# Optimization experiments

Hardware: AMD Instinct MI355X
Metric: run time of the kernel (lower is better)

The kernel has to match this reference:

```python
import jax, jax.numpy as jnp
import numpy as np

N_NODES = 100000
N_EDGES = 1600000
IN_F = 128
HID = 128
OUT_F = 40


def _gcn_conv(x, W, b, src, dst):
    # PyG GCNConv: h = x @ W; out[dst] += norm * h[src]; out += b
    n = x.shape[0]
    h = x @ W  # [N, out_channels]
    deg = jnp.zeros((n,), h.dtype).at[dst].add(jnp.ones((dst.shape[0],), h.dtype))
    dinv = jnp.where(deg > 0, jax.lax.rsqrt(deg), 0.0)  # deg^{-1/2}
    norm = dinv[src] * dinv[dst]  # [E+N]
    msg = h[src] * norm[:, None]  # [E+N, out_channels] gather
    out = jnp.zeros_like(h).at[dst].add(msg)  # scatter-add at targets
    if b is not None:
        out = out + b
    return out


def setup_inputs() -> dict:
    key = jax.random.key(0)
    k_x, k_e, k1, k2, k3, kb1, kb2 = jax.random.split(key, 7)
    x = jax.random.normal(k_x, (N_NODES, IN_F), dtype=jnp.float32)
    edge_index = jax.random.randint(k_e, (2, N_EDGES), 0, N_NODES, dtype=jnp.int64)
    s_in = 1.0 / np.sqrt(IN_F)
    s_h = 1.0 / np.sqrt(HID)
    W_in = jax.random.normal(k1, (IN_F, HID), dtype=jnp.float32) * s_in
    b_in = jnp.zeros((HID,), dtype=jnp.float32)
    W_mid = jax.random.normal(k2, (HID, HID), dtype=jnp.float32) * s_h
    b_mid = jnp.zeros((HID,), dtype=jnp.float32)
    W_out = jax.random.normal(k3, (HID, OUT_F), dtype=jnp.float32) * s_h
    return {"x": x, "edge_index": edge_index, "W_in": W_in, "b_in": b_in,
            "W_mid": W_mid, "b_mid": b_mid, "W_out": W_out}


def reference(x, edge_index, W_in, b_in, W_mid, b_mid, W_out):
    n = x.shape[0]
    loops = jnp.arange(n, dtype=edge_index.dtype)
    src = jnp.concatenate([edge_index[0], loops])  # add self-loops
    dst = jnp.concatenate([edge_index[1], loops])
    h = jax.nn.relu(_gcn_conv(x, W_in, b_in, src, dst))
    h = jax.nn.relu(_gcn_conv(h, W_mid, b_mid, src, dst))
    h = _gcn_conv(h, W_out, None, src, dst)  # out_conv: bias=False
    return jax.nn.log_softmax(h, axis=1)
```

## Files before the change

### kernel.cpp

```cpp
#include <hip/hip_runtime.h>
#include <math.h>

#define N_NODES 100000
#define N_EDGES 1600000
#define NBUCK 391
#define BSTRIDE 4608

typedef __attribute__((ext_vector_type(8))) _Float16 h8v;
typedef __attribute__((ext_vector_type(4))) float f32x4;
typedef __attribute__((ext_vector_type(2))) int i32x2;


__launch_bounds__(256)
__global__ void k_prep(const int* __restrict__ srcv, const int* __restrict__ dstv,
                       int* __restrict__ bcnt, unsigned int* __restrict__ ebuf,
                       const float* __restrict__ W1, const float* __restrict__ W2,
                       const float* __restrict__ W3, _Float16* __restrict__ Wt,
                       _Float16* __restrict__ bufA, _Float16* __restrict__ bufB,
                       _Float16* __restrict__ zbuf) {
    const int tid = threadIdx.x;
    const int bid = blockIdx.x;

    if (bid >= 391) {
        if (bid == 543) {
            if (tid < 128) {
                bufA[(size_t)N_NODES * 128 + tid] = (_Float16)0.f;
                bufB[(size_t)N_NODES * 128 + tid] = (_Float16)0.f;
            }
            if (tid < 64)  zbuf[(size_t)N_NODES * 64 + tid] = (_Float16)0.f;
            return;
        }
        int idx = (bid - 391) * 256 + tid;
        if (idx >= 304 * 128) return;
        int n = idx / 128, k = idx % 128;
        const float* W;
        int ncols, nloc;
        _Float16 *ph, *pl;
        if (n < 128)      { W = W1; ncols = 128; nloc = n;       ph = Wt;                 pl = Wt + 128 * 128; }
        else if (n < 256) { W = W2; ncols = 128; nloc = n - 128; ph = Wt + 2 * 128 * 128; pl = Wt + 3 * 128 * 128; }
        else              { W = W3; ncols = 40;  nloc = n - 256; ph = Wt + 4 * 128 * 128; pl = Wt + 4 * 128 * 128 + 48 * 128; }
        float v = (nloc < ncols) ? W[k * ncols + nloc] : 0.f;
        _Float16 hi = (_Float16)v;
        _Float16 lo = (_Float16)(v - (float)hi);
        ph[nloc * 128 + k] = hi;
        pl[nloc * 128 + k] = lo;
        return;
    }

    __shared__ int hist[NBUCK];
    __shared__ int cur[NBUCK];
    for (int t = tid; t < NBUCK; t += 256) hist[t] = 0;
    __syncthreads();
    const int base = bid * 4096;
#pragma unroll
    for (int i = 0; i < 16; i++) {
        int e = base + i * 256 + tid;
        if (e < N_EDGES) atomicAdd(&hist[dstv[e] >> 8], 1);
    }
    __syncthreads();
    for (int t = tid; t < NBUCK; t += 256)
        if (hist[t]) cur[t] = t * BSTRIDE + atomicAdd(&bcnt[t], hist[t]);
    __syncthreads();
#pragma unroll
    for (int i = 0; i < 16; i++) {
        int e = base + i * 256 + tid;
        if (e < N_EDGES) {
            int d = dstv[e];
            int p = atomicAdd(&cur[d >> 8], 1);
            ebuf[p] = ((unsigned int)srcv[e] << 8) | (unsigned int)(d & 255);
        }
    }
}

__launch_bounds__(256)
__global__ void k_bucket(const unsigned int* __restrict__ ebuf, const int* __restrict__ bcnt,
                         i32x2* __restrict__ rowse, float* __restrict__ dinv,
                         int* __restrict__ colidx) {
    __shared__ int cnt[256];
    __shared__ int s[256];
    __shared__ int cur[256];
    const int tid = threadIdx.x;
    const int b = blockIdx.x;
    const int e0 = b * BSTRIDE;
    const int e1 = e0 + bcnt[b];
    cnt[tid] = 0;
    __syncthreads();
    for (int e = e0 + tid; e < e1; e += 256) atomicAdd(&cnt[ebuf[e] & 255u], 1);
    __syncthreads();
    int v = cnt[tid];
    int x = v;
    s[tid] = x;
    __syncthreads();
    for (int d = 1; d < 256; d <<= 1) {
        int t = (tid >= d) ? s[tid - d] : 0;
        __syncthreads();
        x += t;
        s[tid] = x;
        __syncthreads();
    }
    int start = e0 + x - v;
    int node = b * 256 + tid;
    if (node < N_NODES) {
        i32x2 se;
        se.x = start;
        se.y = start + v;
        rowse[node] = se;
        dinv[node] = rsqrtf((float)(v + 1));
    }
    cur[tid] = start;
    __syncthreads();
    for (int e = e0 + tid; e < e1; e += 256) {
        unsigned int sd = ebuf[e];
        int pos = atomicAdd(&cur[sd & 255u], 1);
        colidx[pos] = (int)(sd >> 8);
    }
}


#define GEMM_GRID 625
#define NTILES 3125

__launch_bounds__(256, 2)
__global__ void k_gemm128_f32(const float* __restrict__ Af,
                              const _Float16* __restrict__ Wthi, const _Float16* __restrict__ Wtlo,
                              const float* __restrict__ dinv, _Float16* __restrict__ out) {
    const int lane = threadIdx.x & 63;
    const int wi = threadIdx.x >> 6;
    const int nb = wi * 32;
    const int nn = lane & 15;
    const int kq = (lane >> 4) * 8;
    const int quad = lane >> 4;

    h8v bh[4][2], bl[4][2];
#pragma unroll
    for (int c = 0; c < 4; c++)
#pragma unroll
        for (int t = 0; t < 2; t++) {
            int off = (nb + t * 16 + nn) * 128 + c * 32 + kq;
            bh[c][t] = *(const h8v*)(Wthi + off);
            bl[c][t] = *(const h8v*)(Wtlo + off);
        }

    for (int rt = blockIdx.x; rt < NTILES; rt += GEMM_GRID) {
        const int r0 = rt * 32;
        f32x4 acc[2][2] = {};
#pragma unroll
        for (int c = 0; c < 4; c++) {
            h8v a[2];
#pragma unroll
            for (int m = 0; m < 2; m++) {
                const float* p = Af + (size_t)(r0 + m * 16 + nn) * 128 + c * 32 + kq;
                float4 p0 = *(const float4*)p;
                float4 p1 = *(const float4*)(p + 4);
                h8v av = {(_Float16)p0.x, (_Float16)p0.y, (_Float16)p0.z, (_Float16)p0.w,
                          (_Float16)p1.x, (_Float16)p1.y, (_Float16)p1.z, (_Float16)p1.w};
                a[m] = av;
            }
#pragma unroll
            for (int m = 0; m < 2; m++)
#pragma unroll
                for (int t = 0; t < 2; t++) {
                    acc[m][t] = __builtin_amdgcn_mfma_f32_16x16x32_f16(a[m], bh[c][t], acc[m][t], 0, 0, 0);
                    acc[m][t] = __builtin_amdgcn_mfma_f32_16x16x32_f16(a[m], bl[c][t], acc[m][t], 0, 0, 0);
                }
        }
#pragma unroll
        for (int m = 0; m < 2; m++)
#pragma unroll
            for (int reg = 0; reg < 4; reg++) {
                int r = r0 + m * 16 + quad * 4 + reg;
                float dv = dinv[r];
#pragma unroll
                for (int t = 0; t < 2; t++)
                    out[(size_t)r * 128 + nb + t * 16 + nn] = (_Float16)(acc[m][t][reg] * dv);
            }
    }
}


__launch_bounds__(256, 2)
__global__ void k_fused128(const _Float16* __restrict__ hp, const i32x2* __restrict__ rowse,
                           const int* __restrict__ colidx, const float* __restrict__ bias,
                           const float* __restrict__ dinv,
                           const _Float16* __restrict__ Wthi, const _Float16* __restrict__ Wtlo,
                           _Float16* __restrict__ out) {
    __shared__ __align__(16) _Float16 As[32 * 128];
    const int lane = threadIdx.x & 63;
    const int wi = threadIdx.x >> 6;
    const int nn = lane & 15;
    const int quad = lane >> 4;
    const int kq = quad * 8;
    const int nb = wi * 32;

    h8v bh[4][2], bl[4][2];
#pragma unroll
    for (int c = 0; c < 4; c++)
#pragma unroll
        for (int t = 0; t < 2; t++) {
            int off = (nb + t * 16 + nn) * 128 + c * 32 + kq;
            bh[c][t] = *(const h8v*)(Wthi + off);
            bl[c][t] = *(const h8v*)(Wtlo + off);
        }

    const int r0 = blockIdx.x * 32;

    const int rs = quad;
    const int cp = nn;
    const _Float16* hpc = hp + cp * 8;
    const float* bp = bias + cp * 8;
    float4 b0 = *(const float4*)bp;
    float4 b1 = *(const float4*)(bp + 4);
    float bb[8] = {b0.x, b0.y, b0.z, b0.w, b1.x, b1.y, b1.z, b1.w};
#pragma unroll
    for (int p = 0; p < 2; p++) {
        const int rl = wi * 8 + p * 4 + rs;
        const int r = r0 + rl;
        const i32x2 se = rowse[r];
        const int deg = se.y - se.x;
        int m = deg;
        m = max(m, __shfl_xor(m, 16));
        m = max(m, __shfl_xor(m, 32));
        h8v acc = {};
        for (int it = 0; it < m; it += 4) {
            int i0 = se.x + it;
            int s0 = colidx[i0];
            int s1 = colidx[i0 + 1];
            int s2 = colidx[i0 + 2];
            int s3 = colidx[i0 + 3];
            s0 = (it < deg) ? s0 : N_NODES;
            s1 = (it + 1 < deg) ? s1 : N_NODES;
            s2 = (it + 2 < deg) ? s2 : N_NODES;
            s3 = (it + 3 < deg) ? s3 : N_NODES;
            h8v v0 = *(const h8v*)(hpc + (size_t)s0 * 128);
            h8v v1 = *(const h8v*)(hpc + (size_t)s1 * 128);
            h8v v2 = *(const h8v*)(hpc + (size_t)s2 * 128);
            h8v v3 = *(const h8v*)(hpc + (size_t)s3 * 128);
            acc += v0;
            acc += v1;
            acc += v2;
            acc += v3;
        }
        h8v sv = *(const h8v*)(hpc + (size_t)r * 128);
        float dv = rsqrtf((float)(deg + 1));
        h8v o;
#pragma unroll
        for (int j = 0; j < 8; j++) {
            float sx = (float)acc[j] + (float)sv[j];
            o[j] = (_Float16)fmaxf(fmaf(dv, sx, bb[j]), 0.f);
        }
        *(h8v*)(As + rl * 128 + ((cp ^ (rl & 15)) * 8)) = o;
    }
    __syncthreads();

    f32x4 acc2[2][2] = {};
#pragma unroll
    for (int c = 0; c < 4; c++) {
        h8v a[2];
#pragma unroll
        for (int mm = 0; mm < 2; mm++) {
            int R = mm * 16 + nn;
            int ch = (c * 4 + quad) ^ (R & 15);
            a[mm] = *(const h8v*)(As + R * 128 + ch * 8);
        }
#pragma unroll
        for (int mm = 0; mm < 2; mm++)
#pragma unroll
            for (int t = 0; t < 2; t++) {
                acc2[mm][t] = __builtin_amdgcn_mfma_f32_16x16x32_f16(a[mm], bh[c][t], acc2[mm][t], 0, 0, 0);
                acc2[mm][t] = __builtin_amdgcn_mfma_f32_16x16x32_f16(a[mm], bl[c][t], acc2[mm][t], 0, 0, 0);
            }
    }
#pragma unroll
    for (int mm = 0; mm < 2; mm++)
#pragma unroll
        for (int reg = 0; reg < 4; reg++) {
            int r = r0 + mm * 16 + quad * 4 + reg;
            float dv = dinv[r];
#pragma unroll
            for (int t = 0; t < 2; t++)
                out[(size_t)r * 128 + nb + t * 16 + nn] = (_Float16)(acc2[mm][t][reg] * dv);
        }
}

__launch_bounds__(256, 2)
__global__ void k_fused40(const _Float16* __restrict__ hp, const i32x2* __restrict__ rowse,
                          const int* __restrict__ colidx, const float* __restrict__ bias,
                          const float* __restrict__ dinv,
                          const _Float16* __restrict__ Wthi, const _Float16* __restrict__ Wtlo,
                          _Float16* __restrict__ out) {
    __shared__ __align__(16) _Float16 As[32 * 128];
    const int lane = threadIdx.x & 63;
    const int wi = threadIdx.x >> 6;
    const int nn = lane & 15;
    const int quad = lane >> 4;
    const int kq = quad * 8;

    h8v bh[4], bl[4];
    if (wi < 3) {
#pragma unroll
        for (int c = 0; c < 4; c++) {
            int off = (wi * 16 + nn) * 128 + c * 32 + kq;
            bh[c] = *(const h8v*)(Wthi + off);
            bl[c] = *(const h8v*)(Wtlo + off);
        }
    }

    const int r0 = blockIdx.x * 32;

    const int rs = quad;
    const int cp = nn;
    const _Float16* hpc = hp + cp * 8;
    const float* bp = bias + cp * 8;
    float4 b0 = *(const float4*)bp;
    float4 b1 = *(const float4*)(bp + 4);
    float bb[8] = {b0.x, b0.y, b0.z, b0.w, b1.x, b1.y, b1.z, b1.w};
#pragma unroll
    for (int p = 0; p < 2; p++) {
        const int rl = wi * 8 + p * 4 + rs;
        const int r = r0 + rl;
        const i32x2 se = rowse[r];
        const int deg = se.y - se.x;
        int m = deg;
        m = max(m, __shfl_xor(m, 16));
        m = max(m, __shfl_xor(m, 32));
        h8v acc = {};
        for (int it = 0; it < m; it += 4) {
            int i0 = se.x + it;
            int s0 = colidx[i0];
            int s1 = colidx[i0 + 1];
            int s2 = colidx[i0 + 2];
            int s3 = colidx[i0 + 3];
            s0 = (it < deg) ? s0 : N_NODES;
            s1 = (it + 1 < deg) ? s1 : N_NODES;
            s2 = (it + 2 < deg) ? s2 : N_NODES;
            s3 = (it + 3 < deg) ? s3 : N_NODES;
            h8v v0 = *(const h8v*)(hpc + (size_t)s0 * 128);
            h8v v1 = *(const h8v*)(hpc + (size_t)s1 * 128);
            h8v v2 = *(const h8v*)(hpc + (size_t)s2 * 128);
            h8v v3 = *(const h8v*)(hpc + (size_t)s3 * 128);
            acc += v0;
            acc += v1;
            acc += v2;
            acc += v3;
        }
        h8v sv = *(const h8v*)(hpc + (size_t)r * 128);
        float dv = rsqrtf((float)(deg + 1));
        h8v o;
#pragma unroll
        for (int j = 0; j < 8; j++) {
            float sx = (float)acc[j] + (float)sv[j];
            o[j] = (_Float16)fmaxf(fmaf(dv, sx, bb[j]), 0.f);
        }
        *(h8v*)(As + rl * 128 + ((cp ^ (rl & 15)) * 8)) = o;
    }
    __syncthreads();

    if (wi < 3) {
        f32x4 acc2[2] = {};
#pragma unroll
        for (int c = 0; c < 4; c++) {
            h8v a[2];
#pragma unroll
            for (int mm = 0; mm < 2; mm++) {
                int R = mm * 16 + nn;
                int ch = (c * 4 + quad) ^ (R & 15);
                a[mm] = *(const h8v*)(As + R * 128 + ch * 8);
            }
#pragma unroll
            for (int mm = 0; mm < 2; mm++) {
                acc2[mm] = __builtin_amdgcn_mfma_f32_16x16x32_f16(a[mm], bh[c], acc2[mm], 0, 0, 0);
                acc2[mm] = __builtin_amdgcn_mfma_f32_16x16x32_f16(a[mm], bl[c], acc2[mm], 0, 0, 0);
            }
        }
#pragma unroll
        for (int mm = 0; mm < 2; mm++)
#pragma unroll
            for (int reg = 0; reg < 4; reg++) {
                int r = r0 + mm * 16 + quad * 4 + reg;
                float dv = dinv[r];
                out[(size_t)r * 64 + wi * 16 + nn] = (_Float16)(acc2[mm][reg] * dv);
            }
    }
}


__launch_bounds__(256)
__global__ void k_agg_out(const _Float16* __restrict__ hp, const i32x2* __restrict__ rowse,
                          const int* __restrict__ colidx, float* __restrict__ out) {
    const int lane = threadIdx.x & 63;
    const int wid = (blockIdx.x * blockDim.x + threadIdx.x) >> 6;
    const int rs = lane >> 3;
    const int cp = lane & 7;
    const int r = wid * 8 + rs;

    const i32x2 se = rowse[r];
    const int deg = se.y - se.x;
    int m = deg;
    m = max(m, __shfl_xor(m, 8));
    m = max(m, __shfl_xor(m, 16));
    m = max(m, __shfl_xor(m, 32));

    const _Float16* hpc = hp + cp * 8;
    h8v acc = {};
    for (int it = 0; it < m; it += 4) {
        int i0 = se.x + it;
        int s0 = colidx[i0];
        int s1 = colidx[i0 + 1];
        int s2 = colidx[i0 + 2];
        int s3 = colidx[i0 + 3];
        s0 = (it < deg) ? s0 : N_NODES;
        s1 = (it + 1 < deg) ? s1 : N_NODES;
        s2 = (it + 2 < deg) ? s2 : N_NODES;
        s3 = (it + 3 < deg) ? s3 : N_NODES;
        h8v v0 = *(const h8v*)(hpc + (size_t)s0 * 64);
        h8v v1 = *(const h8v*)(hpc + (size_t)s1 * 64);
        h8v v2 = *(const h8v*)(hpc + (size_t)s2 * 64);
        h8v v3 = *(const h8v*)(hpc + (size_t)s3 * 64);
        acc += v0;
        acc += v1;
        acc += v2;
        acc += v3;
    }

    h8v sv = *(const h8v*)(hpc + (size_t)r * 64);
    float dv = rsqrtf((float)(deg + 1));
    float z[8];
#pragma unroll
    for (int j = 0; j < 8; j++) z[j] = dv * ((float)acc[j] + (float)sv[j]);

    const bool act = cp < 5;
    float pm = -INFINITY;
    if (act) {
#pragma unroll
        for (int j = 0; j < 8; j++) pm = fmaxf(pm, z[j]);
    }
    pm = fmaxf(pm, __shfl_xor(pm, 1));
    pm = fmaxf(pm, __shfl_xor(pm, 2));
    pm = fmaxf(pm, __shfl_xor(pm, 4));
    float pe = 0.f;
    if (act) {
#pragma unroll
        for (int j = 0; j < 8; j++) pe += __expf(z[j] - pm);
    }
    pe += __shfl_xor(pe, 1);
    pe += __shfl_xor(pe, 2);
    pe += __shfl_xor(pe, 4);
    float lse = __logf(pe);
    if (act) {
        float* po = out + (size_t)r * 40 + cp * 8;
        float4 o0 = make_float4(z[0] - pm - lse, z[1] - pm - lse, z[2] - pm - lse, z[3] - pm - lse);
        float4 o1 = make_float4(z[4] - pm - lse, z[5] - pm - lse, z[6] - pm - lse, z[7] - pm - lse);
        *(float4*)po = o0;
        *(float4*)(po + 4) = o1;
    }
}


extern "C" void kernel_launch(void* const* d_in, const int* in_sizes, int n_in,
                              void* d_out, int out_size, void* d_ws, size_t ws_size,
                              hipStream_t stream) {
    const float* x     = (const float*)d_in[0];
    const int*   ei    = (const int*)d_in[1];
    const float* W_in  = (const float*)d_in[2];
    const float* b_in  = (const float*)d_in[3];
    const float* W_mid = (const float*)d_in[4];
    const float* b_mid = (const float*)d_in[5];
    const float* W_out = (const float*)d_in[6];
    float* out = (float*)d_out;

    const int* srcv = ei;
    const int* dstv = ei + N_EDGES;

    char* w = (char*)d_ws;
    float* dinv   = (float*)(w);
    i32x2* rowse  = (i32x2*)(w + (1ull << 19));
    int* bcnt     = (int*)(w + 1507328);
    int* colidx   = (int*)(w + (2ull << 20));
    unsigned int* ebuf = (unsigned int*)(w + (10ull << 20));
    _Float16* Wt  = (_Float16*)(w + (18ull << 20));
    _Float16* bufA = (_Float16*)(w + (19ull << 20));
    _Float16* bufB = (_Float16*)(w + (45ull << 20));
    _Float16* zbuf = (_Float16*)(w + (71ull << 20));

    _Float16* W1h = Wt;
    _Float16* W1l = Wt + 128 * 128;
    _Float16* W2h = Wt + 2 * 128 * 128;
    _Float16* W2l = Wt + 3 * 128 * 128;
    _Float16* W3h = Wt + 4 * 128 * 128;
    _Float16* W3l = Wt + 4 * 128 * 128 + 48 * 128;

    (void)hipMemsetAsync(bcnt, 0, NBUCK * sizeof(int), stream);
    k_prep<<<544, 256, 0, stream>>>(srcv, dstv, bcnt, ebuf, W_in, W_mid, W_out, Wt, bufA, bufB, zbuf);
    k_bucket<<<NBUCK, 256, 0, stream>>>(ebuf, bcnt, rowse, dinv, colidx);

    k_gemm128_f32<<<GEMM_GRID, 256, 0, stream>>>(x, W1h, W1l, dinv, bufA);
    k_fused128<<<NTILES, 256, 0, stream>>>(bufA, rowse, colidx, b_in, dinv, W2h, W2l, bufB);
    k_fused40<<<NTILES, 256, 0, stream>>>(bufB, rowse, colidx, b_mid, dinv, W3h, W3l, zbuf);
    k_agg_out<<<N_NODES / 32, 256, 0, stream>>>(zbuf, rowse, colidx, out);
}
```

Before: 353.0 us.

## Fold first-layer GEMM into prep kernel and move source scaling into aggregation

The first-layer GEMM on x no longer depends on degree normalisation, so it is merged into the prep kernel as extra blocks. It runs alongside edge bucketing, and one kernel launch is removed. Source-side dinv scaling now happens inside the gather loops, with fp32 accumulation and a zeroed dinv sentinel, instead of in the GEMM epilogues. The fused kernels now use 16-row tiles with weights loaded per block instead of held in registers. This gives more blocks and lower register pressure, at the cost of extra dinv gathers per edge and repeated weight loads.

```diff
diff --git a/kernel.cpp b/kernel.cpp
--- a/kernel.cpp
+++ b/kernel.cpp
@@ -10,19 +10,80 @@
 typedef __attribute__((ext_vector_type(4))) float f32x4;
 typedef __attribute__((ext_vector_type(2))) int i32x2;
 
-
-__launch_bounds__(256)
+#define GEMM_GRID 625
+#define NTILES 3125
+
+
 __global__ void k_prep(const int* __restrict__ srcv, const int* __restrict__ dstv,
                        int* __restrict__ bcnt, unsigned int* __restrict__ ebuf,
-                       const float* __restrict__ W1, const float* __restrict__ W2,
-                       const float* __restrict__ W3, _Float16* __restrict__ Wt,
+                       const float* __restrict__ x, const float* __restrict__ W1,
+                       const float* __restrict__ W2, const float* __restrict__ W3,
+                       _Float16* __restrict__ Wt,
                        _Float16* __restrict__ bufA, _Float16* __restrict__ bufB,
                        _Float16* __restrict__ zbuf) {
     const int tid = threadIdx.x;
     const int bid = blockIdx.x;
 
-    if (bid >= 391) {
-        if (bid == 543) {
+    if (bid < 625) {
+        const int lane = tid & 63;
+        const int wi = tid >> 6;
+        const int nb = wi * 32;
+        const int nn = lane & 15;
+        const int quad = lane >> 4;
+        const int kq = quad * 8;
+
+        h8v bh[4][2], bl[4][2];
+#pragma unroll
+        for (int c = 0; c < 4; c++)
+#pragma unroll
+            for (int t = 0; t < 2; t++) {
+#pragma unroll
+                for (int j = 0; j < 8; j++) {
+                    float w = W1[(c * 32 + kq + j) * 128 + nb + t * 16 + nn];
+                    _Float16 hi = (_Float16)w;
+                    bh[c][t][j] = hi;
+                    bl[c][t][j] = (_Float16)(w - (float)hi);
+                }
+            }
+
+        for (int rt = bid; rt < NTILES; rt += GEMM_GRID) {
+            const int r0 = rt * 32;
+            f32x4 acc[2][2] = {};
+#pragma unroll
+            for (int c = 0; c < 4; c++) {
+                h8v a[2];
+#pragma unroll
+                for (int m = 0; m < 2; m++) {
+                    const float* p = x + (size_t)(r0 + m * 16 + nn) * 128 + c * 32 + kq;
+                    float4 p0 = *(const float4*)p;
+                    float4 p1 = *(const float4*)(p + 4);
+                    h8v av = {(_Float16)p0.x, (_Float16)p0.y, (_Float16)p0.z, (_Float16)p0.w,
+                              (_Float16)p1.x, (_Float16)p1.y, (_Float16)p1.z, (_Float16)p1.w};
+                    a[m] = av;
+                }
+#pragma unroll
+                for (int m = 0; m < 2; m++)
+#pragma unroll
+                    for (int t = 0; t < 2; t++) {
+                        acc[m][t] = __builtin_amdgcn_mfma_f32_16x16x32_f16(a[m], bh[c][t], acc[m][t], 0, 0, 0);
+                        acc[m][t] = __builtin_amdgcn_mfma_f32_16x16x32_f16(a[m], bl[c][t], acc[m][t], 0, 0, 0);
+                    }
+            }
+#pragma unroll
+            for (int m = 0; m < 2; m++)
+#pragma unroll
+                for (int reg = 0; reg < 4; reg++) {
+                    int r = r0 + m * 16 + quad * 4 + reg;
+#pragma unroll
+                    for (int t = 0; t < 2; t++)
+                        bufA[(size_t)r * 128 + nb + t * 16 + nn] = (_Float16)acc[m][t][reg];
+                }
+        }
+        return;
+    }
+
+    if (bid >= 1016) {
+        if (bid == 1104) {
             if (tid < 128) {
                 bufA[(size_t)N_NODES * 128 + tid] = (_Float16)0.f;
                 bufB[(size_t)N_NODES * 128 + tid] = (_Float16)0.f;
@@ -30,20 +91,24 @@
             if (tid < 64)  zbuf[(size_t)N_NODES * 64 + tid] = (_Float16)0.f;
             return;
         }
-        int idx = (bid - 391) * 256 + tid;
-        if (idx >= 304 * 128) return;
+        int idx = (bid - 1016) * 256 + tid;
+        if (idx >= 176 * 128) return;
         int n = idx / 128, k = idx % 128;
-        const float* W;
-        int ncols, nloc;
         _Float16 *ph, *pl;
-        if (n < 128)      { W = W1; ncols = 128; nloc = n;       ph = Wt;                 pl = Wt + 128 * 128; }
-        else if (n < 256) { W = W2; ncols = 128; nloc = n - 128; ph = Wt + 2 * 128 * 128; pl = Wt + 3 * 128 * 128; }
-        else              { W = W3; ncols = 40;  nloc = n - 256; ph = Wt + 4 * 128 * 128; pl = Wt + 4 * 128 * 128 + 48 * 128; }
-        float v = (nloc < ncols) ? W[k * ncols + nloc] : 0.f;
+        float v;
+        if (n < 128) {
+            v = W2[k * 128 + n];
+            ph = Wt + 2 * 128 * 128; pl = Wt + 3 * 128 * 128;
+        } else {
+            int nloc = n - 128;
+            v = (nloc < 40) ? W3[k * 40 + nloc] : 0.f;
+            ph = Wt + 4 * 128 * 128; pl = Wt + 4 * 128 * 128 + 48 * 128;
+            n = nloc;
+        }
         _Float16 hi = (_Float16)v;
         _Float16 lo = (_Float16)(v - (float)hi);
-        ph[nloc * 128 + k] = hi;
-        pl[nloc * 128 + k] = lo;
+        ph[n * 128 + k] = hi;
+        pl[n * 128 + k] = lo;
         return;
     }
 
@@ -51,7 +116,7 @@
     __shared__ int cur[NBUCK];
     for (int t = tid; t < NBUCK; t += 256) hist[t] = 0;
     __syncthreads();
-    const int base = bid * 4096;
+    const int base = (bid - 625) * 4096;
 #pragma unroll
     for (int i = 0; i < 16; i++) {
         int e = base + i * 256 + tid;
@@ -81,6 +146,7 @@
     __shared__ int cur[256];
     const int tid = threadIdx.x;
     const int b = blockIdx.x;
+    if (b == 0 && tid == 0) dinv[N_NODES] = 0.f;
     const int e0 = b * BSTRIDE;
     const int e1 = e0 + bcnt[b];
     cnt[tid] = 0;
@@ -117,110 +183,29 @@
 }
 
 
-#define GEMM_GRID 625
-#define NTILES 3125
-
-__launch_bounds__(256, 2)
-__global__ void k_gemm128_f32(const float* __restrict__ Af,
-                              const _Float16* __restrict__ Wthi, const _Float16* __restrict__ Wtlo,
-                              const float* __restrict__ dinv, _Float16* __restrict__ out) {
-    const int lane = threadIdx.x & 63;
-    const int wi = threadIdx.x >> 6;
-    const int nb = wi * 32;
-    const int nn = lane & 15;
-    const int kq = (lane >> 4) * 8;
-    const int quad = lane >> 4;
-
-    h8v bh[4][2], bl[4][2];
-#pragma unroll
-    for (int c = 0; c < 4; c++)
-#pragma unroll
-        for (int t = 0; t < 2; t++) {
-            int off = (nb + t * 16 + nn) * 128 + c * 32 + kq;
-            bh[c][t] = *(const h8v*)(Wthi + off);
-            bl[c][t] = *(const h8v*)(Wtlo + off);
-        }
-
-    for (int rt = blockIdx.x; rt < NTILES; rt += GEMM_GRID) {
-        const int r0 = rt * 32;
-        f32x4 acc[2][2] = {};
-#pragma unroll
-        for (int c = 0; c < 4; c++) {
-            h8v a[2];
-#pragma unroll
-            for (int m = 0; m < 2; m++) {
-                const float* p = Af + (size_t)(r0 + m * 16 + nn) * 128 + c * 32 + kq;
-                float4 p0 = *(const float4*)p;
-                float4 p1 = *(const float4*)(p + 4);
-                h8v av = {(_Float16)p0.x, (_Float16)p0.y, (_Float16)p0.z, (_Float16)p0.w,
-                          (_Float16)p1.x, (_Float16)p1.y, (_Float16)p1.z, (_Float16)p1.w};
-                a[m] = av;
-            }
-#pragma unroll
-            for (int m = 0; m < 2; m++)
-#pragma unroll
-                for (int t = 0; t < 2; t++) {
-                    acc[m][t] = __builtin_amdgcn_mfma_f32_16x16x32_f16(a[m], bh[c][t], acc[m][t], 0, 0, 0);
-                    acc[m][t] = __builtin_amdgcn_mfma_f32_16x16x32_f16(a[m], bl[c][t], acc[m][t], 0, 0, 0);
-                }
-        }
-#pragma unroll
-        for (int m = 0; m < 2; m++)
-#pragma unroll
-            for (int reg = 0; reg < 4; reg++) {
-                int r = r0 + m * 16 + quad * 4 + reg;
-                float dv = dinv[r];
-#pragma unroll
-                for (int t = 0; t < 2; t++)
-                    out[(size_t)r * 128 + nb + t * 16 + nn] = (_Float16)(acc[m][t][reg] * dv);
-            }
-    }
-}
-
-
-__launch_bounds__(256, 2)
+__launch_bounds__(256)
 __global__ void k_fused128(const _Float16* __restrict__ hp, const i32x2* __restrict__ rowse,
                            const int* __restrict__ colidx, const float* __restrict__ bias,
                            const float* __restrict__ dinv,
                            const _Float16* __restrict__ Wthi, const _Float16* __restrict__ Wtlo,
                            _Float16* __restrict__ out) {
-    __shared__ __align__(16) _Float16 As[32 * 128];
+    __shared__ __align__(16) _Float16 As[16 * 128];
     const int lane = threadIdx.x & 63;
     const int wi = threadIdx.x >> 6;
     const int nn = lane & 15;
     const int quad = lane >> 4;
-    const int kq = quad * 8;
-    const int nb = wi * 32;
-
-    h8v bh[4][2], bl[4][2];
-#pragma unroll
-    for (int c = 0; c < 4; c++)
-#pragma unroll
-        for (int t = 0; t < 2; t++) {
-            int off = (nb + t * 16 + nn) * 128 + c * 32 + kq;
-            bh[c][t] = *(const h8v*)(Wthi + off);
-            bl[c][t] = *(const h8v*)(Wtlo + off);
-        }
-
-    const int r0 = blockIdx.x * 32;
-
-    const int rs = quad;
-    const int cp = nn;
-    const _Float16* hpc = hp + cp * 8;
-    const float* bp = bias + cp * 8;
-    float4 b0 = *(const float4*)bp;
-    float4 b1 = *(const float4*)(bp + 4);
-    float bb[8] = {b0.x, b0.y, b0.z, b0.w, b1.x, b1.y, b1.z, b1.w};
-#pragma unroll
-    for (int p = 0; p < 2; p++) {
-        const int rl = wi * 8 + p * 4 + rs;
+    const int r0 = blockIdx.x * 16;
+
+    {
+        const int rl = wi * 4 + quad;
         const int r = r0 + rl;
         const i32x2 se = rowse[r];
         const int deg = se.y - se.x;
         int m = deg;
         m = max(m, __shfl_xor(m, 16));
         m = max(m, __shfl_xor(m, 32));
-        h8v acc = {};
+        const _Float16* hpc = hp + nn * 8;
+        float accf[8] = {};
         for (int it = 0; it < m; it += 4) {
             int i0 = se.x + it;
             int s0 = colidx[i0];
@@ -231,99 +216,86 @@
             s1 = (it + 1 < deg) ? s1 : N_NODES;
             s2 = (it + 2 < deg) ? s2 : N_NODES;
             s3 = (it + 3 < deg) ? s3 : N_NODES;
+            float d0 = dinv[s0];
+            float d1 = dinv[s1];
+            float d2 = dinv[s2];
+            float d3 = dinv[s3];
             h8v v0 = *(const h8v*)(hpc + (size_t)s0 * 128);
             h8v v1 = *(const h8v*)(hpc + (size_t)s1 * 128);
             h8v v2 = *(const h8v*)(hpc + (size_t)s2 * 128);
             h8v v3 = *(const h8v*)(hpc + (size_t)s3 * 128);
-            acc += v0;
-            acc += v1;
-            acc += v2;
-            acc += v3;
+#pragma unroll
+            for (int j = 0; j < 8; j++) {
+                accf[j] = fmaf(d0, (float)v0[j], accf[j]);
+                accf[j] = fmaf(d1, (float)v1[j], accf[j]);
+                accf[j] = fmaf(d2, (float)v2[j], accf[j]);
+                accf[j] = fmaf(d3, (float)v3[j], accf[j]);
+            }
         }
         h8v sv = *(const h8v*)(hpc + (size_t)r * 128);
         float dv = rsqrtf((float)(deg + 1));
+        const float* bp = bias + nn * 8;
+        float4 b0 = *(const float4*)bp;
+        float4 b1 = *(const float4*)(bp + 4);
+        float bb[8] = {b0.x, b0.y, b0.z, b0.w, b1.x, b1.y, b1.z, b1.w};
         h8v o;
 #pragma unroll
         for (int j = 0; j < 8; j++) {
-            float sx = (float)acc[j] + (float)sv[j];
+            float sx = accf[j] + dv * (float)sv[j];
             o[j] = (_Float16)fmaxf(fmaf(dv, sx, bb[j]), 0.f);
         }
-        *(h8v*)(As + rl * 128 + ((cp ^ (rl & 15)) * 8)) = o;
-    }
-    __syncthreads();
-
-    f32x4 acc2[2][2] = {};
+        *(h8v*)(As + rl * 128 + ((nn ^ rl) * 8)) = o;
+    }
+    __syncthreads();
+
+    const int nb = wi * 32;
+    const int kq = quad * 8;
+    f32x4 acc2[2] = {};
 #pragma unroll
     for (int c = 0; c < 4; c++) {
-        h8v a[2];
-#pragma unroll
-        for (int mm = 0; mm < 2; mm++) {
-            int R = mm * 16 + nn;
-            int ch = (c * 4 + quad) ^ (R & 15);
-            a[mm] = *(const h8v*)(As + R * 128 + ch * 8);
-        }
-#pragma unroll
-        for (int mm = 0; mm < 2; mm++)
-#pragma unroll
-            for (int t = 0; t < 2; t++) {
-                acc2[mm][t] = __builtin_amdgcn_mfma_f32_16x16x32_f16(a[mm], bh[c][t], acc2[mm][t], 0, 0, 0);
-                acc2[mm][t] = __builtin_amdgcn_mfma_f32_16x16x32_f16(a[mm], bl[c][t], acc2[mm][t], 0, 0, 0);
-            }
-    }
-#pragma unroll
-    for (int mm = 0; mm < 2; mm++)
-#pragma unroll
-        for (int reg = 0; reg < 4; reg++) {
-            int r = r0 + mm * 16 + quad * 4 + reg;
-            float dv = dinv[r];
-#pragma unroll
-            for (int t = 0; t < 2; t++)
-                out[(size_t)r * 128 + nb + t * 16 + nn] = (_Float16)(acc2[mm][t][reg] * dv);
-        }
-}
-
-__launch_bounds__(256, 2)
+        int ch = (c * 4 + quad) ^ nn;
+        h8v a = *(const h8v*)(As + nn * 128 + ch * 8);
+#pragma unroll
+        for (int t = 0; t < 2; t++) {
+            int off = (nb + t * 16 + nn) * 128 + c * 32 + kq;
+            h8v bhv = *(const h8v*)(Wthi + off);
+            h8v blv = *(const h8v*)(Wtlo + off);
+            acc2[t] = __builtin_amdgcn_mfma_f32_16x16x32_f16(a, bhv, acc2[t], 0, 0, 0);
+            acc2[t] = __builtin_amdgcn_mfma_f32_16x16x32_f16(a, blv, acc2[t], 0, 0, 0);
+        }
+    }
+#pragma unroll
+    for (int reg = 0; reg < 4; reg++) {
+        int r = r0 + quad * 4 + reg;
+#pragma unroll
+        for (int t = 0; t < 2; t++)
+            out[(size_t)r * 128 + nb + t * 16 + nn] = (_Float16)acc2[t][reg];
+    }
+}
+
+__launch_bounds__(256)
 __global__ void k_fused40(const _Float16* __restrict__ hp, const i32x2* __restrict__ rowse,
                           const int* __restrict__ colidx, const float* __restrict__ bias,
                           const float* __restrict__ dinv,
                           const _Float16* __restrict__ Wthi, const _Float16* __restrict__ Wtlo,
                           _Float16* __restrict__ out) {
-    __shared__ __align__(16) _Float16 As[32 * 128];
+    __shared__ __align__(16) _Float16 As[16 * 128];
     const int lane = threadIdx.x & 63;
     const int wi = threadIdx.x >> 6;
     const int nn = lane & 15;
     const int quad = lane >> 4;
-    const int kq = quad * 8;
-
-    h8v bh[4], bl[4];
-    if (wi < 3) {
-#pragma unroll
-        for (int c = 0; c < 4; c++) {
-            int off = (wi * 16 + nn) * 128 + c * 32 + kq;
-            bh[c] = *(const h8v*)(Wthi + off);
-            bl[c] = *(const h8v*)(Wtlo + off);
-        }
-    }
-
-    const int r0 = blockIdx.x * 32;
-
-    const int rs = quad;
-    const int cp = nn;
-    const _Float16* hpc = hp + cp * 8;
-    const float* bp = bias + cp * 8;
-    float4 b0 = *(const float4*)bp;
-    float4 b1 = *(const float4*)(bp + 4);
-    float bb[8] = {b0.x, b0.y, b0.z, b0.w, b1.x, b1.y, b1.z, b1.w};
-#pragma unroll
-    for (int p = 0; p < 2; p++) {
-        const int rl = wi * 8 + p * 4 + rs;
+    const int r0 = blockIdx.x * 16;
+
+    {
+        const int rl = wi * 4 + quad;
         const int r = r0 + rl;
         const i32x2 se = rowse[r];
         const int deg = se.y - se.x;
         int m = deg;
         m = max(m, __shfl_xor(m, 16));
         m = max(m, __shfl_xor(m, 32));
-        h8v acc = {};
+        const _Float16* hpc = hp + nn * 8;
+        float accf[8] = {};
         for (int it = 0; it < m; it += 4) {
             int i0 = se.x + it;
             int s0 = colidx[i0];
@@ -334,59 +306,64 @@
             s1 = (it + 1 < deg) ? s1 : N_NODES;
             s2 = (it + 2 < deg) ? s2 : N_NODES;
             s3 = (it + 3 < deg) ? s3 : N_NODES;
+            float d0 = dinv[s0];
+            float d1 = dinv[s1];
+            float d2 = dinv[s2];
+            float d3 = dinv[s3];
             h8v v0 = *(const h8v*)(hpc + (size_t)s0 * 128);
             h8v v1 = *(const h8v*)(hpc + (size_t)s1 * 128);
             h8v v2 = *(const h8v*)(hpc + (size_t)s2 * 128);
             h8v v3 = *(const h8v*)(hpc + (size_t)s3 * 128);
-            acc += v0;
-            acc += v1;
-            acc += v2;
-            acc += v3;
+#pragma unroll
+            for (int j = 0; j < 8; j++) {
+                accf[j] = fmaf(d0, (float)v0[j], accf[j]);
+                accf[j] = fmaf(d1, (float)v1[j], accf[j]);
+                accf[j] = fmaf(d2, (float)v2[j], accf[j]);
+                accf[j] = fmaf(d3, (float)v3[j], accf[j]);
+            }
         }
         h8v sv = *(const h8v*)(hpc + (size_t)r * 128);
         float dv = rsqrtf((float)(deg + 1));
+        const float* bp = bias + nn * 8;
+        float4 b0 = *(const float4*)bp;
+        float4 b1 = *(const float4*)(bp + 4);
+        float bb[8] = {b0.x, b0.y, b0.z, b0.w, b1.x, b1.y, b1.z, b1.w};
         h8v o;
 #pragma unroll
         for (int j = 0; j < 8; j++) {
-            float sx = (float)acc[j] + (float)sv[j];
+            float sx = accf[j] + dv * (float)sv[j];
             o[j] = (_Float16)fmaxf(fmaf(dv, sx, bb[j]), 0.f);
         }
-        *(h8v*)(As + rl * 128 + ((cp ^ (rl & 15)) * 8)) = o;
+        *(h8v*)(As + rl * 128 + ((nn ^ rl) * 8)) = o;
     }
     __syncthreads();
 
     if (wi < 3) {
-        f32x4 acc2[2] = {};
+        const int kq = quad * 8;
+        f32x4 acc2 = {};
 #pragma unroll
         for (int c = 0; c < 4; c++) {
-            h8v a[2];
-#pragma unroll
-            for (int mm = 0; mm < 2; mm++) {
-                int R = mm * 16 + nn;
-                int ch = (c * 4 + quad) ^ (R & 15);
-                a[mm] = *(const h8v*)(As + R * 128 + ch * 8);
-            }
-#pragma unroll
-            for (int mm = 0; mm < 2; mm++) {
-                acc2[mm] = __builtin_amdgcn_mfma_f32_16x16x32_f16(a[mm], bh[c], acc2[mm], 0, 0, 0);
-                acc2[mm] = __builtin_amdgcn_mfma_f32_16x16x32_f16(a[mm], bl[c], acc2[mm], 0, 0, 0);
-            }
-        }
-#pragma unroll
-        for (int mm = 0; mm < 2; mm++)
-#pragma unroll
-            for (int reg = 0; reg < 4; reg++) {
-                int r = r0 + mm * 16 + quad * 4 + reg;
-                float dv = dinv[r];
-                out[(size_t)r * 64 + wi * 16 + nn] = (_Float16)(acc2[mm][reg] * dv);
-            }
+            int ch = (c * 4 + quad) ^ nn;
+            h8v a = *(const h8v*)(As + nn * 128 + ch * 8);
+            int off = (wi * 16 + nn) * 128 + c * 32 + kq;
+            h8v bhv = *(const h8v*)(Wthi + off);
+            h8v blv = *(const h8v*)(Wtlo + off);
+            acc2 = __builtin_amdgcn_mfma_f32_16x16x32_f16(a, bhv, acc2, 0, 0, 0);
+            acc2 = __builtin_amdgcn_mfma_f32_16x16x32_f16(a, blv, acc2, 0, 0, 0);
+        }
+#pragma unroll
+        for (int reg = 0; reg < 4; reg++) {
+            int r = r0 + quad * 4 + reg;
+            out[(size_t)r * 64 + wi * 16 + nn] = (_Float16)acc2[reg];
+        }
     }
 }
 
 
 __launch_bounds__(256)
 __global__ void k_agg_out(const _Float16* __restrict__ hp, const i32x2* __restrict__ rowse,
-                          const int* __restrict__ colidx, float* __restrict__ out) {
+                          const int* __restrict__ colidx, const float* __restrict__ dinv,
+                          float* __restrict__ out) {
     const int lane = threadIdx.x & 63;
     const int wid = (blockIdx.x * blockDim.x + threadIdx.x) >> 6;
     const int rs = lane >> 3;
@@ -401,7 +378,7 @@
     m = max(m, __shfl_xor(m, 32));
 
     const _Float16* hpc = hp + cp * 8;
-    h8v acc = {};
+    float accf[8] = {};
     for (int it = 0; it < m; it += 4) {
         int i0 = se.x + it;
         int s0 = colidx[i0];
@@ -412,21 +389,28 @@
         s1 = (it + 1 < deg) ? s1 : N_NODES;
         s2 = (it + 2 < deg) ? s2 : N_NODES;
         s3 = (it + 3 < deg) ? s3 : N_NODES;
+        float d0 = dinv[s0];
+        float d1 = dinv[s1];
+        float d2 = dinv[s2];
+        float d3 = dinv[s3];
         h8v v0 = *(const h8v*)(hpc + (size_t)s0 * 64);
         h8v v1 = *(const h8v*)(hpc + (size_t)s1 * 64);
         h8v v2 = *(const h8v*)(hpc + (size_t)s2 * 64);
         h8v v3 = *(const h8v*)(hpc + (size_t)s3 * 64);
-        acc += v0;
-        acc += v1;
-        acc += v2;
-        acc += v3;
+#pragma unroll
+        for (int j = 0; j < 8; j++) {
+            accf[j] = fmaf(d0, (float)v0[j], accf[j]);
+            accf[j] = fmaf(d1, (float)v1[j], accf[j]);
+            accf[j] = fmaf(d2, (float)v2[j], accf[j]);
+            accf[j] = fmaf(d3, (float)v3[j], accf[j]);
+        }
     }
 
     h8v sv = *(const h8v*)(hpc + (size_t)r * 64);
     float dv = rsqrtf((float)(deg + 1));
     float z[8];
 #pragma unroll
-    for (int j = 0; j < 8; j++) z[j] = dv * ((float)acc[j] + (float)sv[j]);
+    for (int j = 0; j < 8; j++) z[j] = dv * (accf[j] + dv * (float)sv[j]);
 
     const bool act = cp < 5;
     float pm = -INFINITY;
@@ -482,19 +466,17 @@
     _Float16* bufB = (_Float16*)(w + (45ull << 20));
     _Float16* zbuf = (_Float16*)(w + (71ull << 20));
 
-    _Float16* W1h = Wt;
-    _Float16* W1l = Wt + 128 * 128;
     _Float16* W2h = Wt + 2 * 128 * 128;
     _Float16* W2l = Wt + 3 * 128 * 128;
     _Float16* W3h = Wt + 4 * 128 * 128;
     _Float16* W3l = Wt + 4 * 128 * 128 + 48 * 128;
 
     (void)hipMemsetAsync(bcnt, 0, NBUCK * sizeof(int), stream);
-    k_prep<<<544, 256, 0, stream>>>(srcv, dstv, bcnt, ebuf, W_in, W_mid, W_out, Wt, bufA, bufB, zbuf);
+    k_prep<<<1105, 256, 0, stream>>>(srcv, dstv, bcnt, ebuf, x, W_in, W_mid, W_out,
+                                     Wt, bufA, bufB, zbuf);
     k_bucket<<<NBUCK, 256, 0, stream>>>(ebuf, bcnt, rowse, dinv, colidx);
 
-    k_gemm128_f32<<<GEMM_GRID, 256, 0, stream>>>(x, W1h, W1l, dinv, bufA);
-    k_fused128<<<NTILES, 256, 0, stream>>>(bufA, rowse, colidx, b_in, dinv, W2h, W2l, bufB);
-    k_fused40<<<NTILES, 256, 0, stream>>>(bufB, rowse, colidx, b_mid, dinv, W3h, W3l, zbuf);
-    k_agg_out<<<N_NODES / 32, 256, 0, stream>>>(zbuf, rowse, colidx, out);
-}
+    k_fused128<<<N_NODES / 16, 256, 0, stream>>>(bufA, rowse, colidx, b_in, dinv, W2h, W2l, bufB);
+    k_fused40<<<N_NODES / 16, 256, 0, stream>>>(bufB, rowse, colidx, b_mid, dinv, W3h, W3l, zbuf);
+    k_agg_out<<<N_NODES / 32, 256, 0, stream>>>(zbuf, rowse, colidx, dinv, out);
+}
```

New measurement: 347.9 us. Within noise of the previous version (-1.4%).

## Fuse first-layer GEMM into bucket CSR-build kernel, drop separate GEMM launch

Applied to the files above, without the earlier changes.

The layer-1 x@W1 GEMM now runs inside k_bucket. Each of its 391 blocks computes the 256 rows it owns and scales them by dinv taken from shared memory. W1 is split into hi/lo fp16 in registers inside that kernel, so the prep kernel no longer transposes W1 and launches fewer blocks. This removes one kernel launch and the separate dinv/W1 loads. The cost is only 391 blocks doing GEMM work, fewer than the earlier 625-block persistent grid, and higher register pressure in the bucket kernel.

```diff
diff --git a/kernel.cpp b/kernel.cpp
--- a/kernel.cpp
+++ b/kernel.cpp
@@ -10,19 +10,22 @@
 typedef __attribute__((ext_vector_type(4))) float f32x4;
 typedef __attribute__((ext_vector_type(2))) int i32x2;
 
+#define GEMM_GRID 625
+#define NTILES 3125
+
 
 __launch_bounds__(256)
-__global__ void k_prep(const int* __restrict__ srcv, const int* __restrict__ dstv,
-                       int* __restrict__ bcnt, unsigned int* __restrict__ ebuf,
-                       const float* __restrict__ W1, const float* __restrict__ W2,
-                       const float* __restrict__ W3, _Float16* __restrict__ Wt,
-                       _Float16* __restrict__ bufA, _Float16* __restrict__ bufB,
-                       _Float16* __restrict__ zbuf) {
+__global__ void k_bpart(const int* __restrict__ srcv, const int* __restrict__ dstv,
+                        int* __restrict__ bcnt, unsigned int* __restrict__ ebuf,
+                        const float* __restrict__ W2, const float* __restrict__ W3,
+                        _Float16* __restrict__ Wt,
+                        _Float16* __restrict__ bufA, _Float16* __restrict__ bufB,
+                        _Float16* __restrict__ zbuf) {
     const int tid = threadIdx.x;
     const int bid = blockIdx.x;
 
     if (bid >= 391) {
-        if (bid == 543) {
+        if (bid == 479) {
             if (tid < 128) {
                 bufA[(size_t)N_NODES * 128 + tid] = (_Float16)0.f;
                 bufB[(size_t)N_NODES * 128 + tid] = (_Float16)0.f;
@@ -31,19 +34,23 @@
             return;
         }
         int idx = (bid - 391) * 256 + tid;
-        if (idx >= 304 * 128) return;
+        if (idx >= 176 * 128) return;
         int n = idx / 128, k = idx % 128;
-        const float* W;
-        int ncols, nloc;
         _Float16 *ph, *pl;
-        if (n < 128)      { W = W1; ncols = 128; nloc = n;       ph = Wt;                 pl = Wt + 128 * 128; }
-        else if (n < 256) { W = W2; ncols = 128; nloc = n - 128; ph = Wt + 2 * 128 * 128; pl = Wt + 3 * 128 * 128; }
-        else              { W = W3; ncols = 40;  nloc = n - 256; ph = Wt + 4 * 128 * 128; pl = Wt + 4 * 128 * 128 + 48 * 128; }
-        float v = (nloc < ncols) ? W[k * ncols + nloc] : 0.f;
+        float v;
+        if (n < 128) {
+            v = W2[k * 128 + n];
+            ph = Wt + 2 * 128 * 128; pl = Wt + 3 * 128 * 128;
+        } else {
+            int nloc = n - 128;
+            v = (nloc < 40) ? W3[k * 40 + nloc] : 0.f;
+            ph = Wt + 4 * 128 * 128; pl = Wt + 4 * 128 * 128 + 48 * 128;
+            n = nloc;
+        }
         _Float16 hi = (_Float16)v;
         _Float16 lo = (_Float16)(v - (float)hi);
-        ph[nloc * 128 + k] = hi;
-        pl[nloc * 128 + k] = lo;
+        ph[n * 128 + k] = hi;
+        pl[n * 128 + k] = lo;
         return;
     }
 
@@ -72,13 +79,17 @@
     }
 }
 
+
 __launch_bounds__(256)
 __global__ void k_bucket(const unsigned int* __restrict__ ebuf, const int* __restrict__ bcnt,
                          i32x2* __restrict__ rowse, float* __restrict__ dinv,
-                         int* __restrict__ colidx) {
+                         int* __restrict__ colidx,
+                         const float* __restrict__ x, const float* __restrict__ W1,
+                         _Float16* __restrict__ bufA) {
     __shared__ int cnt[256];
     __shared__ int s[256];
     __shared__ int cur[256];
+    __shared__ float sdv[256];
     const int tid = threadIdx.x;
     const int b = blockIdx.x;
     const int e0 = b * BSTRIDE;
@@ -88,24 +99,26 @@
     for (int e = e0 + tid; e < e1; e += 256) atomicAdd(&cnt[ebuf[e] & 255u], 1);
     __syncthreads();
     int v = cnt[tid];
-    int x = v;
-    s[tid] = x;
+    int x0 = v;
+    s[tid] = x0;
     __syncthreads();
     for (int d = 1; d < 256; d <<= 1) {
         int t = (tid >= d) ? s[tid - d] : 0;
         __syncthreads();
-        x += t;
-        s[tid] = x;
+        x0 += t;
+        s[tid] = x0;
         __syncthreads();
     }
-    int start = e0 + x - v;
+    int start = e0 + x0 - v;
     int node = b * 256 + tid;
+    float dvv = rsqrtf((float)(v + 1));
+    sdv[tid] = dvv;
     if (node < N_NODES) {
         i32x2 se;
         se.x = start;
         se.y = start + v;
         rowse[node] = se;
-        dinv[node] = rsqrtf((float)(v + 1));
+        dinv[node] = dvv;
     }
     cur[tid] = start;
     __syncthreads();
@@ -114,42 +127,41 @@
         int pos = atomicAdd(&cur[sd & 255u], 1);
         colidx[pos] = (int)(sd >> 8);
     }
-}
-
-
-#define GEMM_GRID 625
-#define NTILES 3125
-
-__launch_bounds__(256, 2)
-__global__ void k_gemm128_f32(const float* __restrict__ Af,
-                              const _Float16* __restrict__ Wthi, const _Float16* __restrict__ Wtlo,
-                              const float* __restrict__ dinv, _Float16* __restrict__ out) {
-    const int lane = threadIdx.x & 63;
-    const int wi = threadIdx.x >> 6;
+
+    const int lane = tid & 63;
+    const int wi = tid >> 6;
     const int nb = wi * 32;
     const int nn = lane & 15;
-    const int kq = (lane >> 4) * 8;
     const int quad = lane >> 4;
+    const int kq = quad * 8;
 
     h8v bh[4][2], bl[4][2];
 #pragma unroll
     for (int c = 0; c < 4; c++)
 #pragma unroll
         for (int t = 0; t < 2; t++) {
-            int off = (nb + t * 16 + nn) * 128 + c * 32 + kq;
-            bh[c][t] = *(const h8v*)(Wthi + off);
-            bl[c][t] = *(const h8v*)(Wtlo + off);
-        }
-
-    for (int rt = blockIdx.x; rt < NTILES; rt += GEMM_GRID) {
-        const int r0 = rt * 32;
+#pragma unroll
+            for (int j = 0; j < 8; j++) {
+                float w = W1[(c * 32 + kq + j) * 128 + nb + t * 16 + nn];
+                _Float16 hi = (_Float16)w;
+                bh[c][t][j] = hi;
+                bl[c][t][j] = (_Float16)(w - (float)hi);
+            }
+        }
+
+#pragma unroll
+    for (int tile = 0; tile < 8; tile++) {
+        const int r0 = b * 256 + tile * 32;
+        if (r0 >= N_NODES) break;
         f32x4 acc[2][2] = {};
 #pragma unroll
         for (int c = 0; c < 4; c++) {
             h8v a[2];
 #pragma unroll
             for (int m = 0; m < 2; m++) {
-                const float* p = Af + (size_t)(r0 + m * 16 + nn) * 128 + c * 32 + kq;
+                int rl = r0 + m * 16 + nn;
+                rl = (rl < N_NODES) ? rl : (N_NODES - 1);
+                const float* p = x + (size_t)rl * 128 + c * 32 + kq;
                 float4 p0 = *(const float4*)p;
                 float4 p1 = *(const float4*)(p + 4);
                 h8v av = {(_Float16)p0.x, (_Float16)p0.y, (_Float16)p0.z, (_Float16)p0.w,
@@ -169,10 +181,12 @@
 #pragma unroll
             for (int reg = 0; reg < 4; reg++) {
                 int r = r0 + m * 16 + quad * 4 + reg;
-                float dv = dinv[r];
-#pragma unroll
-                for (int t = 0; t < 2; t++)
-                    out[(size_t)r * 128 + nb + t * 16 + nn] = (_Float16)(acc[m][t][reg] * dv);
+                if (r < N_NODES) {
+                    float dv = sdv[r - b * 256];
+#pragma unroll
+                    for (int t = 0; t < 2; t++)
+                        bufA[(size_t)r * 128 + nb + t * 16 + nn] = (_Float16)(acc[m][t][reg] * dv);
+                }
             }
     }
 }
@@ -275,10 +289,10 @@
 #pragma unroll
         for (int reg = 0; reg < 4; reg++) {
             int r = r0 + mm * 16 + quad * 4 + reg;
-            float dv = dinv[r];
+            float dr = dinv[r];
 #pragma unroll
             for (int t = 0; t < 2; t++)
-                out[(size_t)r * 128 + nb + t * 16 + nn] = (_Float16)(acc2[mm][t][reg] * dv);
+                out[(size_t)r * 128 + nb + t * 16 + nn] = (_Float16)(acc2[mm][t][reg] * dr);
         }
 }
 
@@ -377,8 +391,8 @@
 #pragma unroll
             for (int reg = 0; reg < 4; reg++) {
                 int r = r0 + mm * 16 + quad * 4 + reg;
-                float dv = dinv[r];
-                out[(size_t)r * 64 + wi * 16 + nn] = (_Float16)(acc2[mm][reg] * dv);
+                float dr = dinv[r];
+                out[(size_t)r * 64 + wi * 16 + nn] = (_Float16)(acc2[mm][reg] * dr);
             }
     }
 }
@@ -482,18 +496,15 @@
     _Float16* bufB = (_Float16*)(w + (45ull << 20));
     _Float16* zbuf = (_Float16*)(w + (71ull << 20));
 
-    _Float16* W1h = Wt;
-    _Float16* W1l = Wt + 128 * 128;
     _Float16* W2h = Wt + 2 * 128 * 128;
     _Float16* W2l = Wt + 3 * 128 * 128;
     _Float16* W3h = Wt + 4 * 128 * 128;
     _Float16* W3l = Wt + 4 * 128 * 128 + 48 * 128;
 
     (void)hipMemsetAsync(bcnt, 0, NBUCK * sizeof(int), stream);
-    k_prep<<<544, 256, 0, stream>>>(srcv, dstv, bcnt, ebuf, W_in, W_mid, W_out, Wt, bufA, bufB, zbuf);
-    k_bucket<<<NBUCK, 256, 0, stream>>>(ebuf, bcnt, rowse, dinv, colidx);
-
-    k_gemm128_f32<<<GEMM_GRID, 256, 0, stream>>>(x, W1h, W1l, dinv, bufA);
+    k_bpart<<<480, 256, 0, stream>>>(srcv, dstv, bcnt, ebuf, W_mid, W_out, Wt,
+                                     bufA, bufB, zbuf);
+    k_bucket<<<NBUCK, 256, 0, stream>>>(ebuf, bcnt, rowse, dinv, colidx, x, W_in, bufA);
     k_fused128<<<NTILES, 256, 0, stream>>>(bufA, rowse, colidx, b_in, dinv, W2h, W2l, bufB);
     k_fused40<<<NTILES, 256, 0, stream>>>(bufB, rowse, colidx, b_mid, dinv, W3h, W3l, zbuf);
     k_agg_out<<<N_NODES / 32, 256, 0, stream>>>(zbuf, rowse, colidx, out);
```

Result: no change. 350.5 us (-0.7%).
